# Performance work log

Hardware: AMD Instinct MI355X
Metric: run time of the kernel (lower is better)

## Reference

```python
import math
import jax, jax.numpy as jnp
import numpy as np

B, L, D = 2, 2048, 512
H, DK, RANK, NH = 8, 64, 32, 1
K_MAX = 64
BANDWIDTH = 8.0
N_BUCKETS = 16


def setup_inputs() -> dict:
    key = jax.random.key(0)
    ks = jax.random.split(key, 14)
    s = 0.02
    return {
        "query": jax.random.normal(ks[0], (B, L, D), jnp.float32),
        "key": jax.random.normal(ks[1], (B, L, D), jnp.float32),
        "value": jax.random.normal(ks[2], (B, L, D), jnp.float32),
        "Wq": jax.random.normal(ks[3], (D, H * DK), jnp.float32) * s,
        "bq": jnp.zeros((H * DK,), jnp.float32),
        "Wk": jax.random.normal(ks[4], (D, H * DK), jnp.float32) * s,
        "bk": jnp.zeros((H * DK,), jnp.float32),
        "Wv": jax.random.normal(ks[5], (D, H * DK), jnp.float32) * s,
        "bv": jnp.zeros((H * DK,), jnp.float32),
        "U": jax.random.normal(ks[6], (H, DK, RANK), jnp.float32) * s,
        "V": jax.random.normal(ks[7], (H, RANK, D), jnp.float32) * s,
        "rv": jax.random.normal(ks[8], (H, DK, NH), jnp.float32),  # LSH random vectors (buffer)
        "Wo": jax.random.normal(ks[9], (H * D, D), jnp.float32) * s,
        "bo": jnp.zeros((D,), jnp.float32),
    }


def _lsh_hash(x, r):
    # binary quantize then bucketed floor hash: [B,L,dk] @ [dk,nh] -> [B,L,nh]
    xb = (x > 0).astype(x.dtype)
    return jnp.floor((xb @ r) / BANDWIDTH) % N_BUCKETS


def reference(query, key, value, Wq, bq, Wk, bk, Wv, bv, U, V, rv, Wo, bo):
    Bq, Lq, Dm = query.shape
    nheads, dk = U.shape[0], U.shape[1]
    q = (query @ Wq + bq).reshape(Bq, Lq, nheads, dk).transpose(0, 2, 1, 3)  # [B,H,L,dk]
    k = (key @ Wk + bk).reshape(Bq, Lq, nheads, dk).transpose(0, 2, 1, 3)
    v = (value @ Wv + bv).reshape(Bq, Lq, nheads, dk).transpose(0, 2, 1, 3)
    scale = math.sqrt(dk)  # optimized_sqrt(d_key), d_key power of two

    head_outputs = []
    for h in range(nheads):
        qh, kh, vh = q[:, h], k[:, h], v[:, h]  # [B,L,dk]
        qhash = _lsh_hash(qh, rv[h])  # [B,L,nh]
        khash = _lsh_hash(kh, rv[h])
        # [B,L,L] candidate match matrix (all hashes equal)
        matches = (qhash[:, :, None, :] == khash[:, None, :, :]).all(-1)
        # first K_MAX matching key indices in ascending order (== torch nonzero order)
        order = jnp.argsort(jnp.logical_not(matches), axis=-1, stable=True)
        cand = order[:, :, :K_MAX]  # [B,L,k_max]
        valid = jnp.take_along_axis(matches, cand, axis=-1)  # [B,L,k_max]
        ckeys = jnp.take_along_axis(kh[:, None, :, :], cand[..., None], axis=2)  # [B,L,k_max,dk]
        cvals = jnp.take_along_axis(vh[:, None, :, :], cand[..., None], axis=2)
        sim = jnp.einsum('bld,blkd->blk', qh, ckeys) / scale
        sim = jnp.where(valid, sim, -jnp.inf)
        attn = jax.nn.softmax(sim, axis=-1)  # invalid slots get exactly 0 weight
        # attention-weighted sum then low-rank up-projection (linear, so commutes
        # with the weighted sum; avoids the [B,L,k_max,d_model] intermediate)
        ctx = jnp.einsum('blk,blkd->bld', attn, cvals)  # [B,L,dk]
        head_outputs.append((ctx @ U[h]) @ V[h])  # [B,L,d_model]

    concat = jnp.concatenate(head_outputs, axis=-1)  # [B,L,H*d_model]
    return concat @ Wo + bo
```

## Files before the change

### kernel.cpp

```cpp
#include <hip/hip_runtime.h>
#include <math.h>

#define Bb 2
#define Ll 2048
#define Dd 512
#define Hh 8
#define DKq 64
#define NBUCK 16
#define KMAX 64
#define MAX_ITEMS 2304

__device__ __forceinline__ void gl_lds16(const float* g, float* l) {
  __builtin_amdgcn_global_load_lds(
      (const __attribute__((address_space(1))) void*)g,
      (__attribute__((address_space(3))) void*)l, 16, 0, 0);
}

#define VM_WAIT(N)                                                \
  do {                                                            \
    asm volatile("s_waitcnt vmcnt(" #N ")" ::: "memory");         \
    __builtin_amdgcn_sched_barrier(0);                            \
  } while (0)

__global__ __launch_bounds__(64) void proj_kernel(
    const float* __restrict__ Xq, const float* __restrict__ Xk, const float* __restrict__ Xv,
    const float* __restrict__ Wq, const float* __restrict__ Wk, const float* __restrict__ Wv,
    const float* __restrict__ bq, const float* __restrict__ bk, const float* __restrict__ bv,
    float* __restrict__ qb, float* __restrict__ kb, float* __restrict__ vb)
{
  const float *X, *W, *bias; float* dst;
  if (blockIdx.z == 0)      { X=Xq; W=Wq; bias=bq; dst=qb; }
  else if (blockIdx.z == 1) { X=Xk; W=Wk; bias=bk; dst=kb; }
  else                      { X=Xv; W=Wv; bias=bv; dst=vb; }
  __shared__ float As[2][32 * 16];
  __shared__ float Bs[2][16 * 64];
  const int lane = threadIdx.x;
  const int m0 = blockIdx.y * 32;
  const int n0 = blockIdx.x * 64;
  const int tx = lane & 15, ty = lane >> 4;

  const float* aSrc[2];
  #pragma unroll
  for (int j = 0; j < 2; j++) {
    int row  = 16*j + (lane >> 2);
    int key  = (row >> 3) & 3;
    int sK4  = (lane & 3) ^ key;
    aSrc[j] = X + (size_t)(m0 + row) * 512 + (sK4 << 2);
  }
  const float* bSrc[4];
  #pragma unroll
  for (int j = 0; j < 4; j++) {
    int krow = 4*j + (lane >> 4);
    bSrc[j] = W + (size_t)krow * 512 + n0 + ((lane & 15) << 2);
  }

  #pragma unroll
  for (int j = 0; j < 2; j++) gl_lds16(aSrc[j], &As[0][j*256]);
  #pragma unroll
  for (int j = 0; j < 4; j++) gl_lds16(bSrc[j], &Bs[0][j*256]);

  float acc[8][4] = {};
  for (int t = 0; t < 32; t++) {
    const int cur = t & 1;
    if (t < 31) {
      const int ks = (t + 1) * 16;
      const int nb = cur ^ 1;
      #pragma unroll
      for (int j = 0; j < 2; j++) gl_lds16(aSrc[j] + ks,              &As[nb][j*256]);
      #pragma unroll
      for (int j = 0; j < 4; j++) gl_lds16(bSrc[j] + (size_t)ks*512,  &Bs[nb][j*256]);
      VM_WAIT(6);
    } else {
      VM_WAIT(0);
    }

    const float* Ac = &As[cur][0];
    const float* Bc = &Bs[cur][0];
    #pragma unroll
    for (int kk4 = 0; kk4 < 4; kk4++) {
      float4 a[8];
      #pragma unroll
      for (int i = 0; i < 8; i++)
        a[i] = *(const float4*)&Ac[(ty*8 + i)*16 + ((kk4 ^ ty) << 2)];
      #pragma unroll
      for (int s = 0; s < 4; s++) {
        const int kk = kk4*4 + s;
        float4 b0 = *(const float4*)&Bc[kk*64 + tx*4];
        #pragma unroll
        for (int i = 0; i < 8; i++) {
          const float as = (s==0) ? a[i].x : (s==1) ? a[i].y
                         : (s==2) ? a[i].z : a[i].w;
          acc[i][0] += as * b0.x;  acc[i][1] += as * b0.y;
          acc[i][2] += as * b0.z;  acc[i][3] += as * b0.w;
        }
      }
    }
  }

  const int head = n0 >> 6;
  const int d0 = tx * 4;
  #pragma unroll
  for (int i = 0; i < 8; i++) {
    int m = m0 + ty*8 + i;
    int b = m >> 11, l = m & 2047;
    float* drow = &dst[(((size_t)b*Hh + head)*Ll + l)*DKq];
    #pragma unroll
    for (int j = 0; j < 4; j++) drow[d0 + j] = acc[i][j] + bias[n0 + tx*4 + j];
  }
}

__global__ __launch_bounds__(256) void hash_kernel(
    const float* __restrict__ qb, const float* __restrict__ kb,
    const float* __restrict__ rv, int* __restrict__ qhash, int* __restrict__ khash)
{
  int gwave = (blockIdx.x * blockDim.x + threadIdx.x) >> 6;
  int lane = threadIdx.x & 63;
  const int NR = Bb * Hh * Ll;
  if (gwave >= 2 * NR) return;
  int isK = gwave >= NR;
  int row = isK ? gwave - NR : gwave;
  int h = (row >> 11) & 7;
  const float* src = isK ? kb : qb;
  float x = src[(size_t)row * DKq + lane];
  float r = rv[h * DKq + lane];
  float v = (x > 0.0f) ? r : 0.0f;
  #pragma unroll
  for (int off = 32; off; off >>= 1) v += __shfl_xor(v, off);
  if (lane == 0) {
    float fb = floorf(v * 0.125f);
    int ib = (int)fb;
    int bucket = ib & 15;
    (isK ? khash : qhash)[row] = bucket;
  }
}

__global__ __launch_bounds__(64) void kcand_kernel(
    const int* __restrict__ khash, int* __restrict__ kcand, int* __restrict__ kcount)
{
  int bh = blockIdx.x >> 4;
  int bucket = blockIdx.x & 15;
  int lane = threadIdx.x;
  const int* kh = &khash[bh * Ll];
  int* cl = &kcand[(size_t)blockIdx.x * KMAX];
  int total = 0;
  for (int c0 = 0; c0 < Ll && total < KMAX; c0 += 64) {
    int hv = kh[c0 + lane];
    unsigned long long m = __ballot(hv == bucket);
    int pre = __popcll(m & ((1ULL << lane) - 1ULL));
    if (hv == bucket && total + pre < KMAX) cl[total + pre] = c0 + lane;
    total += __popcll(m);
  }
  if (lane == 0) kcount[blockIdx.x] = total < KMAX ? total : KMAX;
}

__global__ __launch_bounds__(256) void qlist_kernel(
    const int* __restrict__ qhash, int* __restrict__ qoff, int* __restrict__ qlist)
{
  int bh = blockIdx.x;
  __shared__ int cnt[NBUCK], cur[NBUCK], off[NBUCK + 1];
  if (threadIdx.x < NBUCK) cnt[threadIdx.x] = 0;
  __syncthreads();
  const int* qh = &qhash[bh * Ll];
  for (int l = threadIdx.x; l < Ll; l += 256) atomicAdd(&cnt[qh[l]], 1);
  __syncthreads();
  if (threadIdx.x == 0) {
    int s = 0;
    for (int i = 0; i < NBUCK; i++) { off[i] = s; cur[i] = s; s += cnt[i]; }
    off[NBUCK] = s;
  }
  __syncthreads();
  if (threadIdx.x < NBUCK + 1) qoff[bh * (NBUCK + 1) + threadIdx.x] = off[threadIdx.x];
  for (int l = threadIdx.x; l < Ll; l += 256) {
    int p = atomicAdd(&cur[qh[l]], 1);
    qlist[bh * Ll + p] = l;
  }
}

__global__ __launch_bounds__(256) void worklist_kernel(
    const int* __restrict__ qoff, const int* __restrict__ kcount,
    int4* __restrict__ items, int* __restrict__ nitems)
{
  int t = threadIdx.x;
  int bh = t >> 4, bucket = t & 15;
  int o0 = qoff[bh * 17 + bucket], o1 = qoff[bh * 17 + bucket + 1];
  int cnt = kcount[t];
  int nq = o1 - o0;
  int n = (cnt > 0) ? ((nq + 15) >> 4) : 0;
  __shared__ int sc[256];
  sc[t] = n;
  __syncthreads();
  for (int off = 1; off < 256; off <<= 1) {
    int v = (t >= off) ? sc[t - off] : 0;
    __syncthreads();
    sc[t] += v;
    __syncthreads();
  }
  int start = sc[t] - n;
  for (int i = 0; i < n; i++) {
    int q0 = 16 * i;
    int qn = nq - q0; if (qn > 16) qn = 16;
    items[start + i] = make_int4(t, o0 + q0, qn, cnt);
  }
  if (t == 255) nitems[0] = sc[255];
}

__device__ __forceinline__ void lds_fence() {
  asm volatile("s_waitcnt lgkmcnt(0)" ::: "memory");
  __builtin_amdgcn_sched_barrier(0);
}

__global__ __launch_bounds__(256, 2) void attn_kernel(
    const float* __restrict__ qb, const float* __restrict__ kb, const float* __restrict__ vb,
    const int* __restrict__ qlist, const int* __restrict__ kcand,
    const int4* __restrict__ items, const int* __restrict__ nitems,
    float* __restrict__ ctx)
{
  __shared__ float qs_all[4][16 * 64];
  __shared__ float sa_all[4][128];
  const int wid = threadIdx.x >> 6, lane = threadIdx.x & 63;
  const int idx = blockIdx.x * 4 + wid;
  if (idx >= nitems[0]) return;
  const int4 it = items[idx];
  const int code = it.x, qstart = it.y, qn = it.z, cnt = it.w;
  const int bh = code >> 4;
  float* qs = qs_all[wid];
  float* sa = sa_all[wid];

  const float* qbh = qb + (size_t)bh * Ll * DKq;
  const float* kbh = kb + (size_t)bh * Ll * DKq;
  const float* vbh = vb + (size_t)bh * Ll * DKq;

  int qidx_v = (lane < qn)  ? qlist[bh * Ll + qstart + lane] : 0;
  int cidx_v = (lane < cnt) ? kcand[(size_t)code * KMAX + lane] : 0;

  float4 kr[16];
  {
    const float4* krow = (const float4*)kbh + (size_t)cidx_v * 16;
    #pragma unroll
    for (int i = 0; i < 16; i++) kr[i] = krow[i];
  }
  float vt[64];
  #pragma unroll
  for (int c = 0; c < 64; c++) {
    int rowc = __shfl(cidx_v, c);
    vt[c] = vbh[(size_t)rowc * DKq + lane];
  }
  #pragma unroll
  for (int i = 0; i < 4; i++) {
    int f = lane + 64 * i;
    int r = f >> 4, c4 = f & 15;
    int qrow = __shfl(qidx_v, r);
    float4 qv = *((const float4*)qbh + (size_t)qrow * 16 + c4);
    *(float4*)&qs[r * 64 + c4 * 4] = qv;
  }
  lds_fence();

  const int b = bh >> 3, h = bh & 7;
  const float4* qs4 = (const float4*)qs;
  const float4* sa4 = (const float4*)sa;

  for (int jj = 0; jj < qn; jj += 2) {
    const int j0  = jj;
    const int j1v = jj + 1;
    const int j1r = (j1v < qn) ? j1v : j0;
    float p00=0.f,p01=0.f,p02=0.f,p03=0.f;
    float p10=0.f,p11=0.f,p12=0.f,p13=0.f;
    #pragma unroll
    for (int i = 0; i < 16; i += 4) {
      float4 qA0 = qs4[j0*16 + i + 0];
      float4 qA1 = qs4[j0*16 + i + 1];
      float4 qA2 = qs4[j0*16 + i + 2];
      float4 qA3 = qs4[j0*16 + i + 3];
      float4 qB0 = qs4[j1r*16 + i + 0];
      float4 qB1 = qs4[j1r*16 + i + 1];
      float4 qB2 = qs4[j1r*16 + i + 2];
      float4 qB3 = qs4[j1r*16 + i + 3];
      p00 += qA0.x*kr[i+0].x + qA0.y*kr[i+0].y + qA0.z*kr[i+0].z + qA0.w*kr[i+0].w;
      p01 += qA1.x*kr[i+1].x + qA1.y*kr[i+1].y + qA1.z*kr[i+1].z + qA1.w*kr[i+1].w;
      p02 += qA2.x*kr[i+2].x + qA2.y*kr[i+2].y + qA2.z*kr[i+2].z + qA2.w*kr[i+2].w;
      p03 += qA3.x*kr[i+3].x + qA3.y*kr[i+3].y + qA3.z*kr[i+3].z + qA3.w*kr[i+3].w;
      p10 += qB0.x*kr[i+0].x + qB0.y*kr[i+0].y + qB0.z*kr[i+0].z + qB0.w*kr[i+0].w;
      p11 += qB1.x*kr[i+1].x + qB1.y*kr[i+1].y + qB1.z*kr[i+1].z + qB1.w*kr[i+1].w;
      p12 += qB2.x*kr[i+2].x + qB2.y*kr[i+2].y + qB2.z*kr[i+2].z + qB2.w*kr[i+2].w;
      p13 += qB3.x*kr[i+3].x + qB3.y*kr[i+3].y + qB3.z*kr[i+3].z + qB3.w*kr[i+3].w;
    }
    float sA = ((p00 + p01) + (p02 + p03)) * 0.125f;
    float sB = ((p10 + p11) + (p12 + p13)) * 0.125f;
    sA = (lane < cnt) ? sA : -INFINITY;
    sB = (lane < cnt) ? sB : -INFINITY;
    float mA = sA, mB = sB;
    #pragma unroll
    for (int off = 32; off; off >>= 1) {
      mA = fmaxf(mA, __shfl_xor(mA, off));
      mB = fmaxf(mB, __shfl_xor(mB, off));
    }
    float eA = __expf(sA - mA);
    float eB = __expf(sB - mB);
    float sumA = eA, sumB = eB;
    #pragma unroll
    for (int off = 32; off; off >>= 1) {
      sumA += __shfl_xor(sumA, off);
      sumB += __shfl_xor(sumB, off);
    }
    lds_fence();
    sa[lane]      = eA;
    sa[64 + lane] = eB;
    lds_fence();
    float c00=0.f,c01=0.f,c02=0.f,c03=0.f;
    float c10=0.f,c11=0.f,c12=0.f,c13=0.f;
    #pragma unroll
    for (int i = 0; i < 16; i++) {
      float4 aA = sa4[i];
      float4 aB = sa4[16 + i];
      c00 += aA.x * vt[4*i + 0];
      c01 += aA.y * vt[4*i + 1];
      c02 += aA.z * vt[4*i + 2];
      c03 += aA.w * vt[4*i + 3];
      c10 += aB.x * vt[4*i + 0];
      c11 += aB.y * vt[4*i + 1];
      c12 += aB.z * vt[4*i + 2];
      c13 += aB.w * vt[4*i + 3];
    }
    {
      float ctxd = ((c00 + c01) + (c02 + c03)) / sumA;
      int qrow = __shfl(qidx_v, j0);
      ctx[((size_t)(b * Ll + qrow)) * 512 + h * 64 + lane] = ctxd;
    }
    if (j1v < qn) {
      float ctxd = ((c10 + c11) + (c12 + c13)) / sumB;
      int qrow = __shfl(qidx_v, j1v);
      ctx[((size_t)(b * Ll + qrow)) * 512 + h * 64 + lane] = ctxd;
    }
  }
}

__global__ __launch_bounds__(256) void uv_kernel(
    const float* __restrict__ U, const float* __restrict__ V, float* __restrict__ T)
{
  int idx = blockIdx.x * 256 + threadIdx.x;
  int n = idx & 511, dk = (idx >> 9) & 63, h = idx >> 15;
  float acc = 0.f;
  #pragma unroll
  for (int r = 0; r < 32; r++)
    acc += U[((size_t)h * 64 + dk) * 32 + r] * V[((size_t)h * 32 + r) * 512 + n];
  T[idx] = acc;
}

__global__ __launch_bounds__(64) void m_kernel(
    const float* __restrict__ T, const float* __restrict__ Wo, float* __restrict__ Mf)
{
  __shared__ float As[2][32 * 16];
  __shared__ float Bs[2][16 * 64];
  const int lane = threadIdx.x;
  const int h  = blockIdx.z;
  const int m0 = blockIdx.y * 32;
  const int n0 = blockIdx.x * 64;
  const int tx = lane & 15, ty = lane >> 4;

  const float* Tb = T + (size_t)h * 64 * 512;
  const float* Wb = Wo + (size_t)h * 512 * 512;

  const float* aSrc[2];
  #pragma unroll
  for (int j = 0; j < 2; j++) {
    int row  = 16*j + (lane >> 2);
    int key  = (row >> 3) & 3;
    int sK4  = (lane & 3) ^ key;
    aSrc[j] = Tb + (size_t)(m0 + row) * 512 + (sK4 << 2);
  }
  const float* bSrc[4];
  #pragma unroll
  for (int j = 0; j < 4; j++) {
    int krow = 4*j + (lane >> 4);
    bSrc[j] = Wb + (size_t)krow * 512 + n0 + ((lane & 15) << 2);
  }

  #pragma unroll
  for (int j = 0; j < 2; j++) gl_lds16(aSrc[j], &As[0][j*256]);
  #pragma unroll
  for (int j = 0; j < 4; j++) gl_lds16(bSrc[j], &Bs[0][j*256]);

  float acc[8][4] = {};
  for (int t = 0; t < 32; t++) {
    const int cur = t & 1;
    if (t < 31) {
      const int ks = (t + 1) * 16;
      const int nb = cur ^ 1;
      #pragma unroll
      for (int j = 0; j < 2; j++) gl_lds16(aSrc[j] + ks,              &As[nb][j*256]);
      #pragma unroll
      for (int j = 0; j < 4; j++) gl_lds16(bSrc[j] + (size_t)ks*512,  &Bs[nb][j*256]);
      VM_WAIT(6);
    } else {
      VM_WAIT(0);
    }

    const float* Ac = &As[cur][0];
    const float* Bc = &Bs[cur][0];
    #pragma unroll
    for (int kk4 = 0; kk4 < 4; kk4++) {
      float4 a[8];
      #pragma unroll
      for (int i = 0; i < 8; i++)
        a[i] = *(const float4*)&Ac[(ty*8 + i)*16 + ((kk4 ^ ty) << 2)];
      #pragma unroll
      for (int s = 0; s < 4; s++) {
        const int kk = kk4*4 + s;
        float4 b0 = *(const float4*)&Bc[kk*64 + tx*4];
        #pragma unroll
        for (int i = 0; i < 8; i++) {
          const float as = (s==0) ? a[i].x : (s==1) ? a[i].y
                         : (s==2) ? a[i].z : a[i].w;
          acc[i][0] += as * b0.x;  acc[i][1] += as * b0.y;
          acc[i][2] += as * b0.z;  acc[i][3] += as * b0.w;
        }
      }
    }
  }

  #pragma unroll
  for (int i = 0; i < 8; i++) {
    int row = h*64 + m0 + ty*8 + i;
    #pragma unroll
    for (int j = 0; j < 4; j++)
      Mf[(size_t)row * 512 + n0 + tx*4 + j] = acc[i][j];
  }
}

__global__ __launch_bounds__(64) void out_gemm(
    const float* __restrict__ A, const float* __restrict__ Bm,
    const float* __restrict__ bias, float* __restrict__ C)
{
  __shared__ float As[2][32 * 16];
  __shared__ float Bs[2][16 * 64];
  const int lane = threadIdx.x;
  const int m0 = blockIdx.y * 32;
  const int n0 = blockIdx.x * 64;
  const int tx = lane & 15, ty = lane >> 4;

  const float* aSrc[2];
  #pragma unroll
  for (int j = 0; j < 2; j++) {
    int row  = 16*j + (lane >> 2);
    int key  = (row >> 3) & 3;
    int sK4  = (lane & 3) ^ key;
    aSrc[j] = A + (size_t)(m0 + row) * 512 + (sK4 << 2);
  }
  const float* bSrc[4];
  #pragma unroll
  for (int j = 0; j < 4; j++) {
    int krow = 4*j + (lane >> 4);
    bSrc[j] = Bm + (size_t)krow * 512 + n0 + ((lane & 15) << 2);
  }

  #pragma unroll
  for (int j = 0; j < 2; j++) gl_lds16(aSrc[j], &As[0][j*256]);
  #pragma unroll
  for (int j = 0; j < 4; j++) gl_lds16(bSrc[j], &Bs[0][j*256]);

  float acc[8][4] = {};
  for (int t = 0; t < 32; t++) {
    const int cur = t & 1;
    if (t < 31) {
      const int ks = (t + 1) * 16;
      const int nb = cur ^ 1;
      #pragma unroll
      for (int j = 0; j < 2; j++) gl_lds16(aSrc[j] + ks,              &As[nb][j*256]);
      #pragma unroll
      for (int j = 0; j < 4; j++) gl_lds16(bSrc[j] + (size_t)ks*512,  &Bs[nb][j*256]);
      VM_WAIT(6);
    } else {
      VM_WAIT(0);
    }

    const float* Ac = &As[cur][0];
    const float* Bc = &Bs[cur][0];
    #pragma unroll
    for (int kk4 = 0; kk4 < 4; kk4++) {
      float4 a[8];
      #pragma unroll
      for (int i = 0; i < 8; i++)
        a[i] = *(const float4*)&Ac[(ty*8 + i)*16 + ((kk4 ^ ty) << 2)];
      #pragma unroll
      for (int s = 0; s < 4; s++) {
        const int kk = kk4*4 + s;
        float4 b0 = *(const float4*)&Bc[kk*64 + tx*4];
        #pragma unroll
        for (int i = 0; i < 8; i++) {
          const float as = (s==0) ? a[i].x : (s==1) ? a[i].y
                         : (s==2) ? a[i].z : a[i].w;
          acc[i][0] += as * b0.x;  acc[i][1] += as * b0.y;
          acc[i][2] += as * b0.z;  acc[i][3] += as * b0.w;
        }
      }
    }
  }

  #pragma unroll
  for (int i = 0; i < 8; i++) {
    int m = m0 + ty*8 + i;
    #pragma unroll
    for (int j = 0; j < 4; j++) {
      int n = n0 + tx*4 + j;
      C[(size_t)m * 512 + n] = acc[i][j] + bias[n];
    }
  }
}

extern "C" void kernel_launch(void* const* d_in, const int* in_sizes, int n_in,
                              void* d_out, int out_size, void* d_ws, size_t ws_size,
                              hipStream_t stream)
{
  const float* query = (const float*)d_in[0];
  const float* key   = (const float*)d_in[1];
  const float* value = (const float*)d_in[2];
  const float* Wq = (const float*)d_in[3];
  const float* bq = (const float*)d_in[4];
  const float* Wk = (const float*)d_in[5];
  const float* bk = (const float*)d_in[6];
  const float* Wv = (const float*)d_in[7];
  const float* bv = (const float*)d_in[8];
  const float* U  = (const float*)d_in[9];
  const float* V  = (const float*)d_in[10];
  const float* rv = (const float*)d_in[11];
  const float* Wo = (const float*)d_in[12];
  const float* bo = (const float*)d_in[13];
  float* out = (float*)d_out;

  float* ws = (float*)d_ws;
  const size_t NQKV = (size_t)Bb * Hh * Ll * DKq;
  float* qb   = ws;
  float* kb   = qb + NQKV;
  float* vb   = kb + NQKV;
  float* ctx  = vb + NQKV;
  float* T    = ctx + NQKV;
  float* Mf   = T + (size_t)Hh * DKq * 512;
  int* qhash  = (int*)(Mf + 512 * 512);
  int* khash  = qhash + Bb * Hh * Ll;
  int* kcand  = khash + Bb * Hh * Ll;
  int* kcount = kcand + Bb * Hh * NBUCK * KMAX;
  int* qoff   = kcount + Bb * Hh * NBUCK;
  int* qlist  = qoff + Bb * Hh * (NBUCK + 1);
  int4* items = (int4*)(qlist + Bb * Hh * Ll);
  int* nitems = (int*)(items + MAX_ITEMS);

  proj_kernel<<<dim3(8, 128, 3), 64, 0, stream>>>(query, key, value,
                                                  Wq, Wk, Wv, bq, bk, bv,
                                                  qb, kb, vb);
  hash_kernel<<<(2 * Bb * Hh * Ll * 64) / 256, 256, 0, stream>>>(qb, kb, rv, qhash, khash);
  kcand_kernel<<<Bb * Hh * NBUCK, 64, 0, stream>>>(khash, kcand, kcount);
  qlist_kernel<<<Bb * Hh, 256, 0, stream>>>(qhash, qoff, qlist);
  worklist_kernel<<<1, 256, 0, stream>>>(qoff, kcount, items, nitems);
  attn_kernel<<<MAX_ITEMS / 4, 256, 0, stream>>>(qb, kb, vb, qlist, kcand,
                                                 items, nitems, ctx);
  uv_kernel<<<(Hh * DKq * 512) / 256, 256, 0, stream>>>(U, V, T);
  m_kernel<<<dim3(8, 2, 8), 64, 0, stream>>>(T, Wo, Mf);
  out_gemm<<<dim3(8, 128), 64, 0, stream>>>(ctx, Mf, bo, out);
}
```

Measured before the change: 252.2 us.

## Fuse bucketing kernels into one and stream projection A rows from global

```diff
diff --git a/kernel.cpp b/kernel.cpp
--- a/kernel.cpp
+++ b/kernel.cpp
@@ -32,56 +32,52 @@
   if (blockIdx.z == 0)      { X=Xq; W=Wq; bias=bq; dst=qb; }
   else if (blockIdx.z == 1) { X=Xk; W=Wk; bias=bk; dst=kb; }
   else                      { X=Xv; W=Wv; bias=bv; dst=vb; }
-  __shared__ float As[2][32 * 16];
-  __shared__ float Bs[2][16 * 64];
+  __shared__ float Bs[3][16 * 64];
   const int lane = threadIdx.x;
   const int m0 = blockIdx.y * 32;
   const int n0 = blockIdx.x * 64;
   const int tx = lane & 15, ty = lane >> 4;
 
-  const float* aSrc[2];
-  #pragma unroll
-  for (int j = 0; j < 2; j++) {
-    int row  = 16*j + (lane >> 2);
-    int key  = (row >> 3) & 3;
-    int sK4  = (lane & 3) ^ key;
-    aSrc[j] = X + (size_t)(m0 + row) * 512 + (sK4 << 2);
-  }
   const float* bSrc[4];
   #pragma unroll
   for (int j = 0; j < 4; j++) {
     int krow = 4*j + (lane >> 4);
     bSrc[j] = W + (size_t)krow * 512 + n0 + ((lane & 15) << 2);
   }
-
-  #pragma unroll
-  for (int j = 0; j < 2; j++) gl_lds16(aSrc[j], &As[0][j*256]);
-  #pragma unroll
-  for (int j = 0; j < 4; j++) gl_lds16(bSrc[j], &Bs[0][j*256]);
+  const float* Arow[8];
+  #pragma unroll
+  for (int i = 0; i < 8; i++) Arow[i] = X + (size_t)(m0 + ty*8 + i) * 512;
+
+  #pragma unroll
+  for (int j = 0; j < 4; j++) gl_lds16(bSrc[j],                  &Bs[0][j*256]);
+  #pragma unroll
+  for (int j = 0; j < 4; j++) gl_lds16(bSrc[j] + (size_t)16*512, &Bs[1][j*256]);
 
   float acc[8][4] = {};
+  int rd = 0, wr = 2;
   for (int t = 0; t < 32; t++) {
-    const int cur = t & 1;
-    if (t < 31) {
-      const int ks = (t + 1) * 16;
-      const int nb = cur ^ 1;
-      #pragma unroll
-      for (int j = 0; j < 2; j++) gl_lds16(aSrc[j] + ks,              &As[nb][j*256]);
-      #pragma unroll
-      for (int j = 0; j < 4; j++) gl_lds16(bSrc[j] + (size_t)ks*512,  &Bs[nb][j*256]);
-      VM_WAIT(6);
-    } else {
-      VM_WAIT(0);
-    }
-
-    const float* Ac = &As[cur][0];
-    const float* Bc = &Bs[cur][0];
+    if (t < 30) {
+      const int ks = (t + 2) * 16;
+      #pragma unroll
+      for (int j = 0; j < 4; j++) gl_lds16(bSrc[j] + (size_t)ks*512, &Bs[wr][j*256]);
+    }
+    if (t == 0)       VM_WAIT(8);
+    else if (t < 30)  VM_WAIT(40);
+    else if (t == 30) VM_WAIT(36);
+    else              VM_WAIT(32);
+
+    const float* Bc = &Bs[rd][0];
+    const int k0 = t * 16;
+    float4 a[8], an[8];
+    #pragma unroll
+    for (int i = 0; i < 8; i++) a[i] = *(const float4*)&Arow[i][k0];
     #pragma unroll
     for (int kk4 = 0; kk4 < 4; kk4++) {
-      float4 a[8];
-      #pragma unroll
-      for (int i = 0; i < 8; i++)
-        a[i] = *(const float4*)&Ac[(ty*8 + i)*16 + ((kk4 ^ ty) << 2)];
+      if (kk4 < 3) {
+        #pragma unroll
+        for (int i = 0; i < 8; i++)
+          an[i] = *(const float4*)&Arow[i][k0 + (kk4 + 1) * 4];
+      }
       #pragma unroll
       for (int s = 0; s < 4; s++) {
         const int kk = kk4*4 + s;
@@ -94,7 +90,13 @@
           acc[i][2] += as * b0.z;  acc[i][3] += as * b0.w;
         }
       }
-    }
+      if (kk4 < 3) {
+        #pragma unroll
+        for (int i = 0; i < 8; i++) a[i] = an[i];
+      }
+    }
+    rd = (rd == 2) ? 0 : rd + 1;
+    wr = (wr == 2) ? 0 : wr + 1;
   }
 
   const int head = n0 >> 6;
@@ -134,74 +136,59 @@
   }
 }
 
-__global__ __launch_bounds__(64) void kcand_kernel(
-    const int* __restrict__ khash, int* __restrict__ kcand, int* __restrict__ kcount)
-{
-  int bh = blockIdx.x >> 4;
-  int bucket = blockIdx.x & 15;
-  int lane = threadIdx.x;
-  const int* kh = &khash[bh * Ll];
-  int* cl = &kcand[(size_t)blockIdx.x * KMAX];
-  int total = 0;
-  for (int c0 = 0; c0 < Ll && total < KMAX; c0 += 64) {
-    int hv = kh[c0 + lane];
-    unsigned long long m = __ballot(hv == bucket);
-    int pre = __popcll(m & ((1ULL << lane) - 1ULL));
-    if (hv == bucket && total + pre < KMAX) cl[total + pre] = c0 + lane;
-    total += __popcll(m);
-  }
-  if (lane == 0) kcount[blockIdx.x] = total < KMAX ? total : KMAX;
-}
-
-__global__ __launch_bounds__(256) void qlist_kernel(
-    const int* __restrict__ qhash, int* __restrict__ qoff, int* __restrict__ qlist)
-{
-  int bh = blockIdx.x;
-  __shared__ int cnt[NBUCK], cur[NBUCK], off[NBUCK + 1];
-  if (threadIdx.x < NBUCK) cnt[threadIdx.x] = 0;
+__global__ __launch_bounds__(256) void bucket_kernel(
+    const int* __restrict__ qhash, const int* __restrict__ khash,
+    int* __restrict__ qlist, int* __restrict__ kcand,
+    int4* __restrict__ items, int* __restrict__ nitems)
+{
+  const int bh = blockIdx.x;
+  const int tid = threadIdx.x;
+  __shared__ int cnt[NBUCK], cur[NBUCK], off[NBUCK + 1], kc[NBUCK];
+  if (tid < NBUCK) cnt[tid] = 0;
   __syncthreads();
   const int* qh = &qhash[bh * Ll];
-  for (int l = threadIdx.x; l < Ll; l += 256) atomicAdd(&cnt[qh[l]], 1);
+  for (int l = tid; l < Ll; l += 256) atomicAdd(&cnt[qh[l]], 1);
   __syncthreads();
-  if (threadIdx.x == 0) {
+  if (tid == 0) {
     int s = 0;
     for (int i = 0; i < NBUCK; i++) { off[i] = s; cur[i] = s; s += cnt[i]; }
     off[NBUCK] = s;
   }
   __syncthreads();
-  if (threadIdx.x < NBUCK + 1) qoff[bh * (NBUCK + 1) + threadIdx.x] = off[threadIdx.x];
-  for (int l = threadIdx.x; l < Ll; l += 256) {
+  for (int l = tid; l < Ll; l += 256) {
     int p = atomicAdd(&cur[qh[l]], 1);
     qlist[bh * Ll + p] = l;
   }
-}
-
-__global__ __launch_bounds__(256) void worklist_kernel(
-    const int* __restrict__ qoff, const int* __restrict__ kcount,
-    int4* __restrict__ items, int* __restrict__ nitems)
-{
-  int t = threadIdx.x;
-  int bh = t >> 4, bucket = t & 15;
-  int o0 = qoff[bh * 17 + bucket], o1 = qoff[bh * 17 + bucket + 1];
-  int cnt = kcount[t];
-  int nq = o1 - o0;
-  int n = (cnt > 0) ? ((nq + 15) >> 4) : 0;
-  __shared__ int sc[256];
-  sc[t] = n;
+  const int lane = tid & 63, w = tid >> 6;
+  const int* kh = &khash[bh * Ll];
+  for (int bi = 0; bi < 4; bi++) {
+    int bucket = w * 4 + bi;
+    int* cl = &kcand[((size_t)bh * NBUCK + bucket) * KMAX];
+    int total = 0;
+    for (int c0 = 0; c0 < Ll && total < KMAX; c0 += 64) {
+      int hv = kh[c0 + lane];
+      unsigned long long mm = __ballot(hv == bucket);
+      int pre = __popcll(mm & ((1ULL << lane) - 1ULL));
+      if (hv == bucket && total + pre < KMAX) cl[total + pre] = c0 + lane;
+      total += __popcll(mm);
+    }
+    if (lane == 0) kc[bucket] = total < KMAX ? total : KMAX;
+  }
   __syncthreads();
-  for (int off = 1; off < 256; off <<= 1) {
-    int v = (t >= off) ? sc[t - off] : 0;
-    __syncthreads();
-    sc[t] += v;
-    __syncthreads();
-  }
-  int start = sc[t] - n;
-  for (int i = 0; i < n; i++) {
-    int q0 = 16 * i;
-    int qn = nq - q0; if (qn > 16) qn = 16;
-    items[start + i] = make_int4(t, o0 + q0, qn, cnt);
-  }
-  if (t == 255) nitems[0] = sc[255];
+  if (tid < NBUCK) {
+    const int bucket = tid;
+    int nq = off[bucket + 1] - off[bucket];
+    int cb = kc[bucket];
+    int n = (cb > 0) ? ((nq + 15) >> 4) : 0;
+    if (n > 0) {
+      int base = atomicAdd(nitems, n);
+      for (int i = 0; i < n; i++) {
+        int q0 = 16 * i;
+        int qn = nq - q0; if (qn > 16) qn = 16;
+        items[base + i] = make_int4(bh * NBUCK + bucket, off[bucket] + q0, qn, cb);
+      }
+    }
+  }
 }
 
 __device__ __forceinline__ void lds_fence() {
@@ -548,9 +535,8 @@
                                                   Wq, Wk, Wv, bq, bk, bv,
                                                   qb, kb, vb);
   hash_kernel<<<(2 * Bb * Hh * Ll * 64) / 256, 256, 0, stream>>>(qb, kb, rv, qhash, khash);
-  kcand_kernel<<<Bb * Hh * NBUCK, 64, 0, stream>>>(khash, kcand, kcount);
-  qlist_kernel<<<Bb * Hh, 256, 0, stream>>>(qhash, qoff, qlist);
-  worklist_kernel<<<1, 256, 0, stream>>>(qoff, kcount, items, nitems);
+  hipMemsetAsync(nitems, 0, sizeof(int), stream);
+  bucket_kernel<<<Bb * Hh, 256, 0, stream>>>(qhash, khash, qlist, kcand, items, nitems);
   attn_kernel<<<MAX_ITEMS / 4, 256, 0, stream>>>(qb, kb, vb, qlist, kcand,
                                                  items, nitems, ctx);
   uv_kernel<<<(Hh * DKq * 512) / 256, 256, 0, stream>>>(U, V, T);
```

New measurement: 274.0 us. 1.09x slower.
